# Kernel optimization log

Hardware: AMD Instinct MI355X
Metric: run time of the kernel (lower is better)

Reference implementation:

```python
import jax, jax.numpy as jnp
import numpy as np

DIM = 32
ED = DIM * DIM          # 1024
HID = ED * 4            # 4096
EPS = 1e-5


def _ln(x, g, b):
    # LayerNorm over last two dims (d, d)
    m = x.mean(axis=(-2, -1), keepdims=True)
    v = jnp.var(x, axis=(-2, -1), keepdims=True)
    return (x - m) * jax.lax.rsqrt(v + EPS) * g + b


def setup_inputs() -> dict:
    key = jax.random.key(0)
    ks = jax.random.split(key, 10)
    b, s, d = 2, 1024, DIM
    inp = {
        "x": jax.random.normal(ks[0], (b, s, d, d), dtype=jnp.float32),
        # StateSpaceLayer params
        "log_A": jax.random.normal(ks[1], (d,), dtype=jnp.float32) * 0.02,
        "w_dt": jax.random.normal(ks[2], (d,), dtype=jnp.float32) / np.sqrt(d),
        "b_dt": jnp.zeros((), dtype=jnp.float32),
        "g_ssm": jnp.ones((d, d), dtype=jnp.float32),
        "b_ssm": jnp.zeros((d, d), dtype=jnp.float32),
        # FFN params
        "g_ffn": jnp.ones((d, d), dtype=jnp.float32),
        "b_ffn": jnp.zeros((d, d), dtype=jnp.float32),
        "W1": jax.random.normal(ks[3], (ED, HID), dtype=jnp.float32) / np.sqrt(ED),
        "bb1": jnp.zeros((HID,), dtype=jnp.float32),
        "W2": jax.random.normal(ks[4], (HID, ED), dtype=jnp.float32) / np.sqrt(HID),
        "bb2": jnp.zeros((ED,), dtype=jnp.float32),
    }
    return inp


def reference(x, log_A, w_dt, b_dt, g_ssm, b_ssm, g_ffn, b_ffn, W1, bb1, W2, bb2):
    b, s, d, _ = x.shape
    # ---- StateSpaceLayer (parallel / training path) ----
    xn = _ln(x, g_ssm, b_ssm)                          # (b,s,d,d)
    A_cont = -jnp.exp(log_A)                           # (d,)
    # dt_proj: Linear(d,1) over last axis, then squeeze -> (b,s,d)
    dt = jax.nn.softplus(jnp.einsum('bsrc,c->bsr', xn, w_dt) + b_dt)
    log_a = dt * A_cont                                # (b,s,d)
    cs = jnp.cumsum(log_a, axis=1)                     # (b,s,d)
    log_M = cs[:, :, None, :] - cs[:, None, :, :]      # (b,t,j,d)
    tmask = jnp.arange(s)[:, None] >= jnp.arange(s)[None, :]  # (t,j) causal
    M = jnp.where(tmask[None, :, :, None], jnp.exp(log_M), 0.0)
    ssm_out = jnp.einsum('btjr,bjrc->btrc', M, xn) + x  # residual
    # ---- MatrixFeedForward ----
    fn = _ln(ssm_out, g_ffn, b_ffn).reshape(b, s, d * d)
    h = jax.nn.gelu(fn @ W1 + bb1, approximate=False)
    y = (h @ W2 + bb2).reshape(b, s, d, d)
    return ssm_out + y
```

## Files before the change

kernel.cpp:

```cpp
#include <hip/hip_runtime.h>
#include <math.h>

#define EPSF 1e-5f

typedef __attribute__((ext_vector_type(4))) float f32x4;
typedef __attribute__((ext_vector_type(4))) int i32x4;
typedef __attribute__((ext_vector_type(8))) int i32x8;

__device__ __forceinline__ unsigned short f2bf(float f) {
  unsigned int u = __float_as_uint(f);
  u += 0x7FFFu + ((u >> 16) & 1u);
  return (unsigned short)(u >> 16);
}
__device__ __forceinline__ float bf2f(unsigned short u) {
  return __uint_as_float((unsigned int)u << 16);
}

__device__ __forceinline__ void async_load16(const void* g, void* l) {
  __builtin_amdgcn_global_load_lds(
      (const __attribute__((address_space(1))) void*)g,
      (__attribute__((address_space(3))) void*)l, 16, 0, 0);
}


__global__ __launch_bounds__(256) void k_ln1(
    const float* __restrict__ x, const float* __restrict__ g, const float* __restrict__ bta,
    const float* __restrict__ w_dt, const float* __restrict__ b_dt,
    const float* __restrict__ log_A, unsigned short* __restrict__ xn,
    float* __restrict__ log_a) {
  __shared__ float red[8];
  int bs = blockIdx.x;
  int t = threadIdx.x;
  float4 v = ((const float4*)(x + (size_t)bs * 1024))[t];
  float s = v.x + v.y + v.z + v.w;
  float ss = v.x * v.x + v.y * v.y + v.z * v.z + v.w * v.w;
  #pragma unroll
  for (int o = 1; o < 64; o <<= 1) { s += __shfl_xor(s, o); ss += __shfl_xor(ss, o); }
  int w = t >> 6;
  if ((t & 63) == 0) { red[w] = s; red[4 + w] = ss; }
  __syncthreads();
  float S = red[0] + red[1] + red[2] + red[3];
  float SS = red[4] + red[5] + red[6] + red[7];
  float m = S * (1.0f / 1024.0f);
  float var = SS * (1.0f / 1024.0f) - m * m;
  float inv = rsqrtf(var + EPSF);
  float4 gv = ((const float4*)g)[t];
  float4 bv = ((const float4*)bta)[t];
  float4 o;
  o.x = (v.x - m) * inv * gv.x + bv.x;
  o.y = (v.y - m) * inv * gv.y + bv.y;
  o.z = (v.z - m) * inv * gv.z + bv.z;
  o.w = (v.w - m) * inv * gv.w + bv.w;
  ushort4 ob;
  ob.x = f2bf(o.x); ob.y = f2bf(o.y); ob.z = f2bf(o.z); ob.w = f2bf(o.w);
  ((ushort4*)(xn + (size_t)bs * 1024))[t] = ob;
  float4 wv = ((const float4*)w_dt)[t & 7];
  float part = o.x * wv.x + o.y * wv.y + o.z * wv.z + o.w * wv.w;
  part += __shfl_xor(part, 1);
  part += __shfl_xor(part, 2);
  part += __shfl_xor(part, 4);
  if ((t & 7) == 0) {
    int r = t >> 3;
    float z = part + b_dt[0];
    float sp = (z > 20.0f) ? z : log1pf(expf(z));
    log_a[(size_t)bs * 32 + r] = sp * (-expf(log_A[r]));
  }
}

template <int PASS, int NKW>
__global__ __launch_bounds__(256) void k_scan_pack(
    const unsigned short* __restrict__ xn, const float* __restrict__ x,
    const float* __restrict__ loga, float4* __restrict__ E, float* __restrict__ P,
    const float* __restrict__ bb2, float* __restrict__ out,
    const float* __restrict__ Wsrc, unsigned char* __restrict__ Wdst, int WC) {
  __shared__ __align__(16) float smem[64 * 65];
  int tid = threadIdx.x;
  if (blockIdx.x >= 512) {
    int bid = blockIdx.x - 512;
    int ncg = WC >> 6;
    int c0 = (bid % ncg) * 64, r0 = (bid / ncg) * 64;
    #pragma unroll
    for (int q = 0; q < 4; ++q) {
      int lin = q * 256 + tid;
      int r = lin >> 4, cq = lin & 15;
      float4 v = *(const float4*)(Wsrc + (size_t)(r0 + r) * WC + c0 + cq * 4);
      smem[r * 65 + cq * 4 + 0] = v.x; smem[r * 65 + cq * 4 + 1] = v.y;
      smem[r * 65 + cq * 4 + 2] = v.z; smem[r * 65 + cq * 4 + 3] = v.w;
    }
    __syncthreads();
    int c = tid & 63, kg = tid >> 6;
    int n = c0 + c;
    int k0 = r0 + kg * 16;
    int pk[4];
    #pragma unroll
    for (int q = 0; q < 4; ++q) {
      int p = __builtin_amdgcn_cvt_pk_fp8_f32(
          smem[(kg * 16 + q * 4 + 0) * 65 + c] * 16.0f,
          smem[(kg * 16 + q * 4 + 1) * 65 + c] * 16.0f, 0, false);
      pk[q] = __builtin_amdgcn_cvt_pk_fp8_f32(
          smem[(kg * 16 + q * 4 + 2) * 65 + c] * 16.0f,
          smem[(kg * 16 + q * 4 + 3) * 65 + c] * 16.0f, p, true);
    }
    size_t sb = (size_t)(n >> 4) * NKW + (k0 >> 7);
    int l = ((k0 >> 5) & 3) * 16 + (n & 15);
    int4 o4; o4.x = pk[0]; o4.y = pk[1]; o4.z = pk[2]; o4.w = pk[3];
    *(int4*)(Wdst + sb * 2048 + ((k0 >> 4) & 1) * 1024 + l * 16) = o4;
    return;
  }
  float* dec = smem;
  float4* sE = (float4*)(smem + 128);
  float* sP = smem + 128 + 1024;
  int bx = blockIdx.x;
  int b = bx >> 8, r = (bx >> 3) & 31, ch = bx & 7;
  int cg = tid & 7, sub = tid >> 3;
  if (tid < 128)
    dec[tid] = expf(loga[(size_t)(b * 1024 + ch * 128 + tid) * 32 + r]);
  __syncthreads();
  int t0 = ch * 128 + sub * 4;
  size_t base = ((size_t)(b * 1024 + t0) * 1024 + r * 32 + cg * 4) >> 2;
  const ushort4* xn4 = (const ushort4*)xn;
  float4 xv[4];
  #pragma unroll
  for (int i = 0; i < 4; ++i) {
    ushort4 u = xn4[base + (size_t)i * 256];
    xv[i].x = bf2f(u.x); xv[i].y = bf2f(u.y); xv[i].z = bf2f(u.z); xv[i].w = bf2f(u.w);
  }
  float4 S = {0.f, 0.f, 0.f, 0.f};
  float Pl = 1.0f;
  #pragma unroll
  for (int i = 0; i < 4; ++i) {
    float d = dec[sub * 4 + i];
    S.x = d * S.x + xv[i].x; S.y = d * S.y + xv[i].y;
    S.z = d * S.z + xv[i].z; S.w = d * S.w + xv[i].w;
    Pl *= d;
  }
  sE[sub * 8 + cg] = S;
  if (cg == 0) sP[sub] = Pl;
  __syncthreads();
  if (PASS == 0) {
    if (tid < 8) {
      float4 Et = {0.f, 0.f, 0.f, 0.f};
      float PP = 1.0f;
      #pragma unroll
      for (int h = 0; h < 32; ++h) {
        float p = sP[h]; float4 e = sE[h * 8 + tid];
        Et.x = p * Et.x + e.x; Et.y = p * Et.y + e.y;
        Et.z = p * Et.z + e.z; Et.w = p * Et.w + e.w;
        PP *= p;
      }
      E[((size_t)(b * 32 + r) * 8 + ch) * 8 + tid] = Et;
      if (tid == 0) P[(b * 32 + r) * 8 + ch] = PP;
    }
  } else {
    float4 Sin = {0.f, 0.f, 0.f, 0.f};
    const float4* Eb = E + (size_t)(b * 32 + r) * 64 + cg;
    const float* Pb = P + (size_t)(b * 32 + r) * 8;
    for (int h = 0; h < ch; ++h) {
      float p = Pb[h]; float4 e = Eb[h * 8];
      Sin.x = p * Sin.x + e.x; Sin.y = p * Sin.y + e.y;
      Sin.z = p * Sin.z + e.z; Sin.w = p * Sin.w + e.w;
    }
    for (int h = 0; h < sub; ++h) {
      float p = sP[h]; float4 e = sE[h * 8 + cg];
      Sin.x = p * Sin.x + e.x; Sin.y = p * Sin.y + e.y;
      Sin.z = p * Sin.z + e.z; Sin.w = p * Sin.w + e.w;
    }
    float4 bb = ((const float4*)bb2)[r * 8 + cg];
    const float4* x4 = (const float4*)x;
    float4* out4 = (float4*)out;
    #pragma unroll
    for (int i = 0; i < 4; ++i) {
      float d = dec[sub * 4 + i];
      Sin.x = d * Sin.x + xv[i].x; Sin.y = d * Sin.y + xv[i].y;
      Sin.z = d * Sin.z + xv[i].z; Sin.w = d * Sin.w + xv[i].w;
      float4 rx = x4[base + (size_t)i * 256];
      float4 oi;
      oi.x = Sin.x + rx.x + bb.x; oi.y = Sin.y + rx.y + bb.y;
      oi.z = Sin.z + rx.z + bb.z; oi.w = Sin.w + rx.w + bb.w;
      out4[base + (size_t)i * 256] = oi;
    }
  }
}

__global__ __launch_bounds__(256) void k_ln2(
    const float* __restrict__ out, const float* __restrict__ bb2,
    const float* __restrict__ g, const float* __restrict__ bta,
    unsigned char* __restrict__ fn) {
  __shared__ __align__(16) unsigned char sC[16384];
  int tid = threadIdx.x;
  int t15 = tid >> 4;
  int kc = tid & 15;
  int tok = (blockIdx.x << 4) + t15;
  const float4* row = (const float4*)(out + (size_t)tok * 1024);
  const float4* b4 = (const float4*)bb2;
  float4 v[16];
  float s = 0.f, ss = 0.f;
  #pragma unroll
  for (int ci = 0; ci < 4; ++ci) {
    int cc = kc + ci * 16;
    #pragma unroll
    for (int q = 0; q < 4; ++q) {
      float4 xv = row[cc * 4 + q];
      float4 bb = b4[cc * 4 + q];
      xv.x -= bb.x; xv.y -= bb.y; xv.z -= bb.z; xv.w -= bb.w;
      v[ci * 4 + q] = xv;
      s += xv.x + xv.y + xv.z + xv.w;
      ss += xv.x * xv.x + xv.y * xv.y + xv.z * xv.z + xv.w * xv.w;
    }
  }
  #pragma unroll
  for (int o = 1; o < 16; o <<= 1) { s += __shfl_xor(s, o); ss += __shfl_xor(ss, o); }
  float m = s * (1.0f / 1024.0f);
  float var = ss * (1.0f / 1024.0f) - m * m;
  float inv = rsqrtf(var + EPSF);
  #pragma unroll
  for (int ci = 0; ci < 4; ++ci) {
    int cc = kc + ci * 16;
    int pk[4];
    #pragma unroll
    for (int q = 0; q < 4; ++q) {
      float4 gv = ((const float4*)g)[cc * 4 + q];
      float4 bv = ((const float4*)bta)[cc * 4 + q];
      float4 xv = v[ci * 4 + q];
      float f0 = (xv.x - m) * inv * gv.x + bv.x;
      float f1 = (xv.y - m) * inv * gv.y + bv.y;
      float f2 = (xv.z - m) * inv * gv.z + bv.z;
      float f3 = (xv.w - m) * inv * gv.w + bv.w;
      int p = __builtin_amdgcn_cvt_pk_fp8_f32(f0, f1, 0, false);
      pk[q] = __builtin_amdgcn_cvt_pk_fp8_f32(f2, f3, p, true);
    }
    int loc = (cc >> 3) * 2048 + (cc & 1) * 1024 + (((cc >> 1) & 3) * 16 + t15) * 16;
    loc ^= ((loc >> 8) & 7) << 4;
    int4 o4; o4.x = pk[0]; o4.y = pk[1]; o4.z = pk[2]; o4.w = pk[3];
    *(int4*)(sC + loc) = o4;
  }
  __syncthreads();
  unsigned char* dst = fn + (size_t)blockIdx.x * 16384;
  #pragma unroll
  for (int p = 0; p < 4; ++p) {
    int a = (p * 256 + tid) * 16;
    int sa = a ^ (((a >> 8) & 7) << 4);
    *(int4*)(dst + a) = *(const int4*)(sC + sa);
  }
}

__global__ __launch_bounds__(256, 2) void k_gemm1(
    const unsigned char* __restrict__ Ap, const unsigned char* __restrict__ Bp,
    const float* __restrict__ bias, unsigned char* __restrict__ C8) {
  __shared__ __align__(16) unsigned char sAB[65536];
  int L = blockIdx.x;
  int xcd = L & 7;
  int nq = xcd & 3, mh = xcd >> 2;
  int rest = L >> 3;
  int nx = rest & 7, my = rest >> 3;
  int n0 = (nq * 8 + nx) * 128;
  int m0 = (mh * 8 + my) * 128;
  int tid = threadIdx.x;
  int wave = tid >> 6, lane = tid & 63;
  int wr = wave >> 1, wc = wave & 1;
  int l15 = lane & 15, quad = lane >> 4;

  f32x4 zero = {0.0f, 0.0f, 0.0f, 0.0f};
  f32x4 acc[4][4];
  #pragma unroll
  for (int i = 0; i < 4; ++i)
    #pragma unroll
    for (int j = 0; j < 4; ++j) acc[i][j] = zero;

  const unsigned char* gsrc = (wave < 2) ? Ap : Bp;
  int rt0 = (wave < 2) ? (m0 >> 4) : (n0 >> 4);
  int aoff = (wave < 2) ? 0 : 16384;
  int w01 = wave & 1;

  #pragma unroll
  for (int t = 0; t < 8; ++t) {
    int idx = w01 * 8 + t, rt = idx >> 1, h = idx & 1;
    async_load16(gsrc + ((size_t)(rt0 + rt) * 8 + 0) * 2048 + h * 1024 + lane * 16,
                 sAB + aoff + rt * 2048 + h * 1024 + lane * 16);
  }

  #pragma unroll 1
  for (int st = 0; st < 8; ++st) {
    int cur = (st & 1) * 32768;
    if (st < 7) {
      int nxt = cur ^ 32768;
      #pragma unroll
      for (int t = 0; t < 8; ++t) {
        int idx = w01 * 8 + t, rt = idx >> 1, h = idx & 1;
        async_load16(gsrc + ((size_t)(rt0 + rt) * 8 + st + 1) * 2048 + h * 1024 + lane * 16,
                     sAB + nxt + aoff + rt * 2048 + h * 1024 + lane * 16);
      }
      asm volatile("s_waitcnt vmcnt(8)" ::: "memory");
    } else {
      asm volatile("s_waitcnt vmcnt(0)" ::: "memory");
    }
    __builtin_amdgcn_s_barrier();
    const unsigned char* sA = sAB + cur;
    const unsigned char* sB = sAB + cur + 16384;
    i32x8 af[4], bf[4];
    #pragma unroll
    for (int i = 0; i < 4; ++i) {
      const unsigned char* pa = sA + (wr * 4 + i) * 2048 + lane * 16;
      i32x4 lo = *(const i32x4*)pa;
      i32x4 hi = *(const i32x4*)(pa + 1024);
      af[i] = __builtin_shufflevector(lo, hi, 0, 1, 2, 3, 4, 5, 6, 7);
    }
    #pragma unroll
    for (int j = 0; j < 4; ++j) {
      const unsigned char* pb = sB + (wc * 4 + j) * 2048 + lane * 16;
      i32x4 lo = *(const i32x4*)pb;
      i32x4 hi = *(const i32x4*)(pb + 1024);
      bf[j] = __builtin_shufflevector(lo, hi, 0, 1, 2, 3, 4, 5, 6, 7);
    }
    #pragma unroll
    for (int i = 0; i < 4; ++i)
      #pragma unroll
      for (int j = 0; j < 4; ++j)
        acc[i][j] = __builtin_amdgcn_mfma_scale_f32_16x16x128_f8f6f4(
            af[i], bf[j], acc[i][j], 0, 0, 0, 0x7F7F7F7F, 0, 0x7F7F7F7F);
    asm volatile("s_waitcnt lgkmcnt(0)" ::: "memory");
    __builtin_amdgcn_s_barrier();
  }

  unsigned char* sC = sAB;
  #pragma unroll
  for (int i = 0; i < 4; ++i) {
    #pragma unroll
    for (int j = 0; j < 4; ++j) {
      int col_l = wc * 64 + j * 16 + l15;
      float bval = bias[n0 + col_l];
      int half2 = (col_l >> 4) & 1, lb = (col_l >> 5) & 3;
      unsigned char* ld = sC + (wr * 4 + i) * 2048 + half2 * 1024 +
                          (lb * 16 + quad * 4) * 16 + l15;
      float vv[4];
      #pragma unroll
      for (int v = 0; v < 4; ++v) {
        float val = acc[i][j][v] * 0.0625f + bval;
        float u = val * (0.7978845608f + 0.035677408f * val * val);
        vv[v] = val / (1.0f + __expf(-2.0f * u));
      }
      int p01 = __builtin_amdgcn_cvt_pk_fp8_f32(vv[0], vv[1], 0, false);
      int p23 = __builtin_amdgcn_cvt_pk_fp8_f32(vv[2], vv[3], 0, false);
      ld[0 * 16] = (unsigned char)(p01 & 0xff);
      ld[1 * 16] = (unsigned char)((p01 >> 8) & 0xff);
      ld[2 * 16] = (unsigned char)(p23 & 0xff);
      ld[3 * 16] = (unsigned char)((p23 >> 8) & 0xff);
    }
  }
  __syncthreads();
  int mt2_0 = m0 >> 4, kp2 = n0 >> 7;
  #pragma unroll
  for (int p = 0; p < 4; ++p) {
    int ci = p * 256 + tid;
    int s = ci >> 7, off = (ci & 127) * 16;
    *(int4*)(C8 + ((size_t)(mt2_0 + s) * 32 + kp2) * 2048 + off) =
        *(const int4*)(sC + s * 2048 + off);
  }
}

__global__ __launch_bounds__(256, 2) void k_gemm2(
    const unsigned char* __restrict__ Ap, const unsigned char* __restrict__ Bp,
    float* __restrict__ O) {
  __shared__ __align__(16) unsigned char sAB[65536];
  int L = blockIdx.x;
  int xcd = L & 7;
  int mq = xcd >> 1, nh = xcd & 1;
  int rest = L >> 3;
  int nx = rest & 7, my = rest >> 3;
  int n0 = (nh * 8 + nx) * 64;
  int m0 = (mq * 8 + my) * 64;
  int tid = threadIdx.x;
  int wave = tid >> 6, lane = tid & 63;
  int wr = wave >> 1, wc = wave & 1;
  int l15 = lane & 15, quad = lane >> 4;

  f32x4 zero = {0.0f, 0.0f, 0.0f, 0.0f};
  f32x4 acc[2][2];
  #pragma unroll
  for (int i = 0; i < 2; ++i)
    #pragma unroll
    for (int j = 0; j < 2; ++j) acc[i][j] = zero;

  const unsigned char* gsrc = (wave < 2) ? Ap : Bp;
  int rt0 = (wave < 2) ? (m0 >> 4) : (n0 >> 4);
  int aoff = (wave < 2) ? 0 : 16384;
  int w01 = wave & 1;

  #pragma unroll
  for (int t = 0; t < 8; ++t) {
    int idx = w01 * 8 + t, sb = idx >> 1, h = idx & 1;
    int rt = sb >> 1, kt = sb & 1;
    async_load16(gsrc + ((size_t)(rt0 + rt) * 32 + kt) * 2048 + h * 1024 + lane * 16,
                 sAB + aoff + sb * 2048 + h * 1024 + lane * 16);
  }

  #pragma unroll 1
  for (int st = 0; st < 16; ++st) {
    int cur = (st & 1) * 32768;
    if (st < 15) {
      int nxt = cur ^ 32768;
      #pragma unroll
      for (int t = 0; t < 8; ++t) {
        int idx = w01 * 8 + t, sb = idx >> 1, h = idx & 1;
        int rt = sb >> 1, kt = sb & 1;
        async_load16(
            gsrc + ((size_t)(rt0 + rt) * 32 + (st + 1) * 2 + kt) * 2048 + h * 1024 + lane * 16,
            sAB + nxt + aoff + sb * 2048 + h * 1024 + lane * 16);
      }
      asm volatile("s_waitcnt vmcnt(8)" ::: "memory");
    } else {
      asm volatile("s_waitcnt vmcnt(0)" ::: "memory");
    }
    __builtin_amdgcn_s_barrier();
    const unsigned char* sA = sAB + cur;
    const unsigned char* sB = sAB + cur + 16384;
    #pragma unroll
    for (int kl = 0; kl < 2; ++kl) {
      i32x8 af[2], bf[2];
      #pragma unroll
      for (int i = 0; i < 2; ++i) {
        const unsigned char* pa = sA + ((wr * 2 + i) * 2 + kl) * 2048 + lane * 16;
        i32x4 lo = *(const i32x4*)pa;
        i32x4 hi = *(const i32x4*)(pa + 1024);
        af[i] = __builtin_shufflevector(lo, hi, 0, 1, 2, 3, 4, 5, 6, 7);
      }
      #pragma unroll
      for (int j = 0; j < 2; ++j) {
        const unsigned char* pb = sB + ((wc * 2 + j) * 2 + kl) * 2048 + lane * 16;
        i32x4 lo = *(const i32x4*)pb;
        i32x4 hi = *(const i32x4*)(pb + 1024);
        bf[j] = __builtin_shufflevector(lo, hi, 0, 1, 2, 3, 4, 5, 6, 7);
      }
      #pragma unroll
      for (int i = 0; i < 2; ++i)
        #pragma unroll
        for (int j = 0; j < 2; ++j)
          acc[i][j] = __builtin_amdgcn_mfma_scale_f32_16x16x128_f8f6f4(
              af[i], bf[j], acc[i][j], 0, 0, 0, 0x7F7F7F7F, 0, 0x7F7F7F7F);
    }
    asm volatile("s_waitcnt lgkmcnt(0)" ::: "memory");
    __builtin_amdgcn_s_barrier();
  }

  #pragma unroll
  for (int i = 0; i < 2; ++i)
    #pragma unroll
    for (int j = 0; j < 2; ++j) {
      int col = n0 + wc * 32 + j * 16 + l15;
      #pragma unroll
      for (int v = 0; v < 4; ++v) {
        int row = m0 + wr * 32 + i * 16 + quad * 4 + v;
        float* p = &O[(size_t)row * 1024 + col];
        *p = *p + acc[i][j][v] * 0.0625f;
      }
    }
}

extern "C" void kernel_launch(void* const* d_in, const int* in_sizes, int n_in,
                              void* d_out, int out_size, void* d_ws, size_t ws_size,
                              hipStream_t stream) {
  const float* x     = (const float*)d_in[0];
  const float* log_A = (const float*)d_in[1];
  const float* w_dt  = (const float*)d_in[2];
  const float* b_dt  = (const float*)d_in[3];
  const float* g_ssm = (const float*)d_in[4];
  const float* b_ssm = (const float*)d_in[5];
  const float* g_ffn = (const float*)d_in[6];
  const float* b_ffn = (const float*)d_in[7];
  const float* W1    = (const float*)d_in[8];
  const float* bb1   = (const float*)d_in[9];
  const float* W2    = (const float*)d_in[10];
  const float* bb2   = (const float*)d_in[11];
  float* out = (float*)d_out;

  const size_t MB = 1u << 20;
  char* ws = (char*)d_ws;
  unsigned short* xn   = (unsigned short*)(ws);
  unsigned char* W1t   = (unsigned char*)(ws + 4 * MB);
  float* loga          = (float*)(ws + 8 * MB);
  float4* Ebuf         = (float4*)(ws + 8 * MB + 262144);
  float* Pbuf          = (float*)(ws + 8 * MB + 393216);
  unsigned char* fn    = (unsigned char*)(ws + 9 * MB);
  unsigned char* W2t   = (unsigned char*)(ws + 11 * MB);
  unsigned char* hbf   = (unsigned char*)(ws + 15 * MB);

  k_ln1<<<2048, 256, 0, stream>>>(x, g_ssm, b_ssm, w_dt, b_dt, log_A, xn, loga);
  k_scan_pack<0, 8><<<1536, 256, 0, stream>>>(xn, x, loga, Ebuf, Pbuf, bb2, out,
                                              W1, W1t, 4096);
  k_scan_pack<1, 32><<<1536, 256, 0, stream>>>(xn, x, loga, Ebuf, Pbuf, bb2, out,
                                               W2, W2t, 1024);
  k_ln2<<<128, 256, 0, stream>>>(out, bb2, g_ffn, b_ffn, fn);
  k_gemm1<<<512, 256, 0, stream>>>(fn, W1t, bb1, hbf);
  k_gemm2<<<512, 256, 0, stream>>>(hbf, W2t, out);
}
```

Measured before the change: 149.0 us.

## Fuse two-pass chunked scan into single kernel with inter-block flag sync

Merges the two scan+weight-pack launches into one kernel. Each scan block publishes its chunk summary (E, P) and sets a flag, then spins until all earlier chunks in the same row have published before finishing the carry-in pass. The weight-pack blocks for W1 and W2 share the same launch. This removes one kernel launch and the recomputation of the local chunk scan, but adds a memset and relies on earlier chunk blocks being scheduled first, since a blocked waiter could otherwise spin forever. The GEMM loop also loads A fragments per row inside the MFMA loop instead of all up front, to lower register pressure.

```diff
diff --git a/kernel.cpp b/kernel.cpp
--- a/kernel.cpp
+++ b/kernel.cpp
@@ -22,6 +22,39 @@
       (__attribute__((address_space(3))) void*)l, 16, 0, 0);
 }
 
+
+__device__ __forceinline__ void pack_tile(
+    const float* __restrict__ Wsrc, unsigned char* __restrict__ Wdst,
+    int WC, int NKW, int bid, int tid, float* smem) {
+  int ncg = WC >> 6;
+  int c0 = (bid % ncg) * 64, r0 = (bid / ncg) * 64;
+  #pragma unroll
+  for (int q = 0; q < 4; ++q) {
+    int lin = q * 256 + tid;
+    int r = lin >> 4, cq = lin & 15;
+    float4 v = *(const float4*)(Wsrc + (size_t)(r0 + r) * WC + c0 + cq * 4);
+    smem[r * 65 + cq * 4 + 0] = v.x; smem[r * 65 + cq * 4 + 1] = v.y;
+    smem[r * 65 + cq * 4 + 2] = v.z; smem[r * 65 + cq * 4 + 3] = v.w;
+  }
+  __syncthreads();
+  int c = tid & 63, kg = tid >> 6;
+  int n = c0 + c;
+  int k0 = r0 + kg * 16;
+  int pk[4];
+  #pragma unroll
+  for (int q = 0; q < 4; ++q) {
+    int p = __builtin_amdgcn_cvt_pk_fp8_f32(
+        smem[(kg * 16 + q * 4 + 0) * 65 + c] * 16.0f,
+        smem[(kg * 16 + q * 4 + 1) * 65 + c] * 16.0f, 0, false);
+    pk[q] = __builtin_amdgcn_cvt_pk_fp8_f32(
+        smem[(kg * 16 + q * 4 + 2) * 65 + c] * 16.0f,
+        smem[(kg * 16 + q * 4 + 3) * 65 + c] * 16.0f, p, true);
+  }
+  size_t sb = (size_t)(n >> 4) * NKW + (k0 >> 7);
+  int l = ((k0 >> 5) & 3) * 16 + (n & 15);
+  int4 o4; o4.x = pk[0]; o4.y = pk[1]; o4.z = pk[2]; o4.w = pk[3];
+  *(int4*)(Wdst + sb * 2048 + ((k0 >> 4) & 1) * 1024 + l * 16) = o4;
+}
 
 __global__ __launch_bounds__(256) void k_ln1(
     const float* __restrict__ x, const float* __restrict__ g, const float* __restrict__ bta,
@@ -67,50 +100,25 @@
   }
 }
 
-template <int PASS, int NKW>
-__global__ __launch_bounds__(256) void k_scan_pack(
+__global__ __launch_bounds__(256) void k_scanf(
     const unsigned short* __restrict__ xn, const float* __restrict__ x,
     const float* __restrict__ loga, float4* __restrict__ E, float* __restrict__ P,
     const float* __restrict__ bb2, float* __restrict__ out,
-    const float* __restrict__ Wsrc, unsigned char* __restrict__ Wdst, int WC) {
+    const float* __restrict__ W1, unsigned char* __restrict__ W1t,
+    const float* __restrict__ W2, unsigned char* __restrict__ W2t,
+    int* __restrict__ flags) {
   __shared__ __align__(16) float smem[64 * 65];
   int tid = threadIdx.x;
-  if (blockIdx.x >= 512) {
-    int bid = blockIdx.x - 512;
-    int ncg = WC >> 6;
-    int c0 = (bid % ncg) * 64, r0 = (bid / ncg) * 64;
-    #pragma unroll
-    for (int q = 0; q < 4; ++q) {
-      int lin = q * 256 + tid;
-      int r = lin >> 4, cq = lin & 15;
-      float4 v = *(const float4*)(Wsrc + (size_t)(r0 + r) * WC + c0 + cq * 4);
-      smem[r * 65 + cq * 4 + 0] = v.x; smem[r * 65 + cq * 4 + 1] = v.y;
-      smem[r * 65 + cq * 4 + 2] = v.z; smem[r * 65 + cq * 4 + 3] = v.w;
-    }
-    __syncthreads();
-    int c = tid & 63, kg = tid >> 6;
-    int n = c0 + c;
-    int k0 = r0 + kg * 16;
-    int pk[4];
-    #pragma unroll
-    for (int q = 0; q < 4; ++q) {
-      int p = __builtin_amdgcn_cvt_pk_fp8_f32(
-          smem[(kg * 16 + q * 4 + 0) * 65 + c] * 16.0f,
-          smem[(kg * 16 + q * 4 + 1) * 65 + c] * 16.0f, 0, false);
-      pk[q] = __builtin_amdgcn_cvt_pk_fp8_f32(
-          smem[(kg * 16 + q * 4 + 2) * 65 + c] * 16.0f,
-          smem[(kg * 16 + q * 4 + 3) * 65 + c] * 16.0f, p, true);
-    }
-    size_t sb = (size_t)(n >> 4) * NKW + (k0 >> 7);
-    int l = ((k0 >> 5) & 3) * 16 + (n & 15);
-    int4 o4; o4.x = pk[0]; o4.y = pk[1]; o4.z = pk[2]; o4.w = pk[3];
-    *(int4*)(Wdst + sb * 2048 + ((k0 >> 4) & 1) * 1024 + l * 16) = o4;
+  int bx = blockIdx.x;
+  if (bx >= 512) {
+    int bid = bx - 512;
+    if (bid < 1024) pack_tile(W1, W1t, 4096, 8, bid, tid, smem);
+    else            pack_tile(W2, W2t, 1024, 32, bid - 1024, tid, smem);
     return;
   }
   float* dec = smem;
   float4* sE = (float4*)(smem + 128);
   float* sP = smem + 128 + 1024;
-  int bx = blockIdx.x;
   int b = bx >> 8, r = (bx >> 3) & 31, ch = bx & 7;
   int cg = tid & 7, sub = tid >> 3;
   if (tid < 128)
@@ -137,21 +145,30 @@
   sE[sub * 8 + cg] = S;
   if (cg == 0) sP[sub] = Pl;
   __syncthreads();
-  if (PASS == 0) {
-    if (tid < 8) {
-      float4 Et = {0.f, 0.f, 0.f, 0.f};
-      float PP = 1.0f;
-      #pragma unroll
-      for (int h = 0; h < 32; ++h) {
-        float p = sP[h]; float4 e = sE[h * 8 + tid];
-        Et.x = p * Et.x + e.x; Et.y = p * Et.y + e.y;
-        Et.z = p * Et.z + e.z; Et.w = p * Et.w + e.w;
-        PP *= p;
-      }
-      E[((size_t)(b * 32 + r) * 8 + ch) * 8 + tid] = Et;
-      if (tid == 0) P[(b * 32 + r) * 8 + ch] = PP;
-    }
-  } else {
+  if (tid < 8) {
+    float4 Et = {0.f, 0.f, 0.f, 0.f};
+    float PP = 1.0f;
+    #pragma unroll
+    for (int h = 0; h < 32; ++h) {
+      float p = sP[h]; float4 e = sE[h * 8 + tid];
+      Et.x = p * Et.x + e.x; Et.y = p * Et.y + e.y;
+      Et.z = p * Et.z + e.z; Et.w = p * Et.w + e.w;
+      PP *= p;
+    }
+    E[((size_t)(b * 32 + r) * 8 + ch) * 8 + tid] = Et;
+    if (tid == 0) P[(b * 32 + r) * 8 + ch] = PP;
+    __threadfence();
+  }
+  __syncthreads();
+  int lkbase = (b * 32 + r) * 8;
+  if (tid == 0) {
+    atomicExch(&flags[lkbase + ch], 1);
+    for (int h = 0; h < ch; ++h)
+      while (atomicAdd(&flags[lkbase + h], 0) == 0) {}
+    __threadfence();
+  }
+  __syncthreads();
+  {
     float4 Sin = {0.f, 0.f, 0.f, 0.f};
     const float4* Eb = E + (size_t)(b * 32 + r) * 64 + cg;
     const float* Pb = P + (size_t)(b * 32 + r) * 8;
@@ -297,14 +314,7 @@
     __builtin_amdgcn_s_barrier();
     const unsigned char* sA = sAB + cur;
     const unsigned char* sB = sAB + cur + 16384;
-    i32x8 af[4], bf[4];
-    #pragma unroll
-    for (int i = 0; i < 4; ++i) {
-      const unsigned char* pa = sA + (wr * 4 + i) * 2048 + lane * 16;
-      i32x4 lo = *(const i32x4*)pa;
-      i32x4 hi = *(const i32x4*)(pa + 1024);
-      af[i] = __builtin_shufflevector(lo, hi, 0, 1, 2, 3, 4, 5, 6, 7);
-    }
+    i32x8 bf[4];
     #pragma unroll
     for (int j = 0; j < 4; ++j) {
       const unsigned char* pb = sB + (wc * 4 + j) * 2048 + lane * 16;
@@ -313,11 +323,16 @@
       bf[j] = __builtin_shufflevector(lo, hi, 0, 1, 2, 3, 4, 5, 6, 7);
     }
     #pragma unroll
-    for (int i = 0; i < 4; ++i)
+    for (int i = 0; i < 4; ++i) {
+      const unsigned char* pa = sA + (wr * 4 + i) * 2048 + lane * 16;
+      i32x4 lo = *(const i32x4*)pa;
+      i32x4 hi = *(const i32x4*)(pa + 1024);
+      i32x8 a = __builtin_shufflevector(lo, hi, 0, 1, 2, 3, 4, 5, 6, 7);
       #pragma unroll
       for (int j = 0; j < 4; ++j)
         acc[i][j] = __builtin_amdgcn_mfma_scale_f32_16x16x128_f8f6f4(
-            af[i], bf[j], acc[i][j], 0, 0, 0, 0x7F7F7F7F, 0, 0x7F7F7F7F);
+            a, bf[j], acc[i][j], 0, 0, 0, 0x7F7F7F7F, 0, 0x7F7F7F7F);
+    }
     asm volatile("s_waitcnt lgkmcnt(0)" ::: "memory");
     __builtin_amdgcn_s_barrier();
   }
@@ -480,15 +495,15 @@
   float* loga          = (float*)(ws + 8 * MB);
   float4* Ebuf         = (float4*)(ws + 8 * MB + 262144);
   float* Pbuf          = (float*)(ws + 8 * MB + 393216);
+  int* flags           = (int*)(ws + 8 * MB + 409600);
   unsigned char* fn    = (unsigned char*)(ws + 9 * MB);
   unsigned char* W2t   = (unsigned char*)(ws + 11 * MB);
   unsigned char* hbf   = (unsigned char*)(ws + 15 * MB);
 
+  hipMemsetAsync(flags, 0, 4096, stream);
   k_ln1<<<2048, 256, 0, stream>>>(x, g_ssm, b_ssm, w_dt, b_dt, log_A, xn, loga);
-  k_scan_pack<0, 8><<<1536, 256, 0, stream>>>(xn, x, loga, Ebuf, Pbuf, bb2, out,
-                                              W1, W1t, 4096);
-  k_scan_pack<1, 32><<<1536, 256, 0, stream>>>(xn, x, loga, Ebuf, Pbuf, bb2, out,
-                                               W2, W2t, 1024);
+  k_scanf<<<2560, 256, 0, stream>>>(xn, x, loga, Ebuf, Pbuf, bb2, out,
+                                    W1, W1t, W2, W2t, flags);
   k_ln2<<<128, 256, 0, stream>>>(out, bb2, g_ffn, b_ffn, fn);
   k_gemm1<<<512, 256, 0, stream>>>(fn, W1t, bb1, hbf);
   k_gemm2<<<512, 256, 0, stream>>>(hbf, W2t, out);
```

Result: slower. 183.6 us (+23.3%).
